# Optimization experiments

Measured on AMD Instinct MI355X. Metric: run time of the kernel, lower is better.

Reference implementation:

```python
import jax, jax.numpy as jnp
import numpy as np

B, LQ, LK, D = 8, 2048, 2048, 1024


def setup_inputs() -> dict:
    key = jax.random.key(0)
    k1, k2, k3, k4, k5 = jax.random.split(key, 5)
    inp = jax.random.normal(k1, (B, LQ, D), dtype=jnp.float32)
    memory = jax.random.normal(k2, (B, LK, D), dtype=jnp.float32)
    # 0/1 float mask over memory positions (1 = masked out)
    mask = (jax.random.uniform(k3, (B, LK)) < 0.15).astype(jnp.float32)
    # nn.Linear(D, 1, bias=False): weight shape [1, D], kaiming-uniform-ish init
    w_input = jax.random.uniform(k4, (1, D), dtype=jnp.float32,
                                 minval=-1.0 / np.sqrt(D), maxval=1.0 / np.sqrt(D))
    # dot_scale ~ U(0, 1/sqrt(D)) per original .uniform_(1/input_size**0.5)
    dot_scale = jax.random.uniform(k5, (D,), dtype=jnp.float32,
                                   minval=0.0, maxval=1.0 / np.sqrt(D))
    return {"input": inp, "memory": memory, "mask": mask,
            "w_input": w_input, "dot_scale": dot_scale}


def reference(input, memory, mask, w_input, dot_scale):
    # input_dot: Linear(D,1,bias=False) -> [B, Lq, 1]
    input_dot = jnp.einsum('bqd,od->bqo', input, w_input)  # o == 1
    # cross_dot: (input * dot_scale) @ memory^T -> [B, Lq, Lk]
    cross_dot = jnp.einsum('bqd,bkd->bqk', input * dot_scale, memory)
    att = input_dot + cross_dot - 1e30 * mask[:, None, :]
    weight_one = jax.nn.softmax(att, axis=-1)  # [B, Lq, Lk]
    output_one = jnp.einsum('bqk,bkd->bqd', weight_one, memory)
    return output_one
```

## Files before the change

### kernel.cpp

```cpp
#include <hip/hip_runtime.h>

#define B_  8
#define LQ_ 2048
#define LK_ 2048
#define D_  1024

typedef unsigned short u16;
using short8  = __attribute__((ext_vector_type(8))) short;
using floatx4 = __attribute__((ext_vector_type(4))) float;

#define GAS __attribute__((address_space(1)))
#define LAS __attribute__((address_space(3)))

__device__ __forceinline__ u16 f2bf(float f) {
  unsigned u = __float_as_uint(f);
  u += 0x7fffu + ((u >> 16) & 1u);
  return (u16)(u >> 16);
}
__device__ __forceinline__ float bf2f(u16 h) {
  return __uint_as_float(((unsigned)h) << 16);
}

__global__ void prep(const float* __restrict__ in, const float* __restrict__ mem,
                     const float* __restrict__ ds, u16* __restrict__ qb,
                     u16* __restrict__ mb, u16* __restrict__ mbT,
                     float* __restrict__ denom) {
  __shared__ u16 tile[64][68];
  int tid = threadIdx.x;
  int tx = tid & 15, ty = tid >> 4;
  int b = blockIdx.z;

  if (denom && blockIdx.y == 16 && blockIdx.x == 0 && blockIdx.z == 0) {
    float4 z = {0.f, 0.f, 0.f, 0.f};
    float4* d4 = (float4*)denom;
#pragma unroll
    for (int i = 0; i < (B_ * LQ_ / 4) / 256; i++)
      d4[tid + i * 256] = z;
  }

  if (blockIdx.y < 16) {
    int k0 = blockIdx.x * 64, d0 = blockIdx.y * 64;
    const float* mB = mem + (size_t)b * LK_ * D_;
    u16* mbB = mb  + (size_t)b * LK_ * D_;
    u16* mtB = mbT + (size_t)b * D_ * LK_;
#pragma unroll
    for (int i = 0; i < 4; i++) {
      int r = ty + 16 * i;
      float4 v = *(const float4*)(mB + (size_t)(k0 + r) * D_ + d0 + tx * 4);
      ushort4 h;
      h.x = f2bf(v.x); h.y = f2bf(v.y); h.z = f2bf(v.z); h.w = f2bf(v.w);
      *(ushort4*)(mbB + (size_t)(k0 + r) * D_ + d0 + tx * 4) = h;
      *(ushort4*)(&tile[r][tx * 4]) = h;
    }
    __syncthreads();
#pragma unroll
    for (int i = 0; i < 4; i++) {
      int rr = ty + 16 * i;
      ushort4 o;
      o.x = tile[tx * 4 + 0][rr];
      o.y = tile[tx * 4 + 1][rr];
      o.z = tile[tx * 4 + 2][rr];
      o.w = tile[tx * 4 + 3][rr];
      *(ushort4*)(mtB + (size_t)(d0 + rr) * LK_ + k0 + tx * 4) = o;
    }
  } else {
    int q0 = blockIdx.x * 64, d0 = (blockIdx.y - 16) * 64;
    const float* iB = in + (size_t)b * LQ_ * D_;
    u16* qB = qb + (size_t)b * LQ_ * D_;
    float4 s4 = *(const float4*)(ds + d0 + tx * 4);
#pragma unroll
    for (int i = 0; i < 4; i++) {
      int r = ty + 16 * i;
      float4 v = *(const float4*)(iB + (size_t)(q0 + r) * D_ + d0 + tx * 4);
      ushort4 h;
      h.x = f2bf(v.x * s4.x); h.y = f2bf(v.y * s4.y);
      h.z = f2bf(v.z * s4.z); h.w = f2bf(v.w * s4.w);
      *(ushort4*)(qB + (size_t)(q0 + r) * D_ + d0 + tx * 4) = h;
    }
  }
}

template <int MODE>
__global__ __launch_bounds__(512, 2) void gemm_bt(
    const u16* __restrict__ A, const u16* __restrict__ Bm,
    void* __restrict__ C, const float* __restrict__ mask,
    float* __restrict__ denom, int K, int ld, int ldc,
    size_t sA, size_t sB, size_t sC) {
  __shared__ __align__(16) u16 As[4 * 8192];
  __shared__ __align__(16) u16 Bs[4 * 8192];

  const int tid = threadIdx.x;
  const int lane = tid & 63, w = tid >> 6;
  const int lm = lane & 15, quad = (lane >> 4) & 3;
  const int wm = (w >> 2) * 128, wn = (w & 3) * 64;

  const int tiles_n = gridDim.x;
  int bid = (blockIdx.z * gridDim.y + blockIdx.y) * tiles_n + blockIdx.x;
  int bz = bid & 7;
  int s = bid >> 3;
  const int GM = 4;
  int per_group = GM * tiles_n;
  int group = s / per_group;
  int rem = s - group * per_group;
  int tm = group * GM + (rem & (GM - 1));
  int tn = rem >> 2;

  const u16* Ab = A  + (size_t)bz * sA + (size_t)(tm * 256) * ld;
  const u16* Bb = Bm + (size_t)bz * sB + (size_t)(tn * 256) * ld;

  int goff[2], ldst[2];
#pragma unroll
  for (int j = 0; j < 2; j++) {
    int c = tid + 512 * j;
    int row = c >> 2;
    int slot = (c & 3) ^ ((row >> 1) & 3);
    goff[j] = row * ld + slot * 8;
    ldst[j] = c * 8;
  }

  const int sw = quad ^ ((lm >> 1) & 3);
  const int aoff = (wm + lm) * 32 + sw * 8;
  const int boff = (wn + lm) * 32 + sw * 8;

  auto stageA = [&](int koff, int plane) {
#pragma unroll
    for (int j = 0; j < 2; j++)
      __builtin_amdgcn_global_load_lds((GAS void*)(Ab + goff[j] + koff),
                                       (LAS void*)(As + (plane << 13) + ldst[j]),
                                       16, 0, 0);
  };
  auto stageB = [&](int koff, int plane) {
#pragma unroll
    for (int j = 0; j < 2; j++)
      __builtin_amdgcn_global_load_lds((GAS void*)(Bb + goff[j] + koff),
                                       (LAS void*)(Bs + (plane << 13) + ldst[j]),
                                       16, 0, 0);
  };

  floatx4 acc[8][4];
#pragma unroll
  for (int i = 0; i < 8; i++)
#pragma unroll
    for (int j = 0; j < 4; j++)
      acc[i][j] = {0.f, 0.f, 0.f, 0.f};

  float rs[8] = {0.f, 0.f, 0.f, 0.f, 0.f, 0.f, 0.f, 0.f};
  short8 bf[4];

#define DS_PHASE(MH, KK, CUR, STG)                                            \
  {                                                                           \
    const u16* Ap = As + (((CUR) * 2 + (KK)) << 13);                          \
    if ((MH) == 0) {                                                          \
      const u16* Bp = Bs + (((CUR) * 2 + (KK)) << 13);                        \
      _Pragma("unroll")                                                       \
      for (int ni = 0; ni < 4; ni++)                                          \
        bf[ni] = *(const short8*)(Bp + boff + ni * 512);                      \
    }                                                                         \
    short8 af[4];                                                             \
    _Pragma("unroll")                                                         \
    for (int m = 0; m < 4; m++)                                               \
      af[m] = *(const short8*)(Ap + aoff + ((MH) * 4 + m) * 512);             \
    STG;                                                                      \
    if constexpr (MODE == 2) {                                                \
      _Pragma("unroll")                                                       \
      for (int m = 0; m < 4; m++) {                                           \
        uint4 u = *(const uint4*)&af[m];                                      \
        rs[(MH) * 4 + m] +=                                                   \
            __uint_as_float(u.x << 16) + __uint_as_float(u.x & 0xffff0000u)   \
          + __uint_as_float(u.y << 16) + __uint_as_float(u.y & 0xffff0000u)   \
          + __uint_as_float(u.z << 16) + __uint_as_float(u.z & 0xffff0000u)   \
          + __uint_as_float(u.w << 16) + __uint_as_float(u.w & 0xffff0000u);  \
      }                                                                       \
    }                                                                         \
    __builtin_amdgcn_s_setprio(1);                                            \
    _Pragma("unroll")                                                         \
    for (int m = 0; m < 4; m++)                                               \
      _Pragma("unroll")                                                       \
      for (int ni = 0; ni < 4; ni++)                                          \
        acc[(MH) * 4 + m][ni] = __builtin_amdgcn_mfma_f32_16x16x32_bf16(      \
            af[m], bf[ni], acc[(MH) * 4 + m][ni], 0, 0, 0);                   \
    __builtin_amdgcn_s_setprio(0);                                            \
  }

  const int NT = K >> 6;
  stageA(0, 0); stageB(0, 0); stageA(32, 1); stageB(32, 1);

  for (int t = 0; t < NT; ++t) {
    const int cur = t & 1, nb = cur ^ 1;
    const bool have = (t + 1 < NT);
    const int k0n = (t + 1) << 6;

    asm volatile("s_waitcnt vmcnt(4)" ::: "memory");
    __builtin_amdgcn_sched_barrier(0);
    __builtin_amdgcn_s_barrier();

    DS_PHASE(0, 0, cur, if (have) stageA(k0n, nb * 2))
    DS_PHASE(1, 0, cur, if (have) stageB(k0n, nb * 2))

    if (have) { asm volatile("s_waitcnt vmcnt(4)" ::: "memory"); }
    else      { asm volatile("s_waitcnt vmcnt(0)" ::: "memory"); }
    __builtin_amdgcn_sched_barrier(0);
    __builtin_amdgcn_s_barrier();

    DS_PHASE(0, 1, cur, if (have) stageA(k0n + 32, nb * 2 + 1))
    DS_PHASE(1, 1, cur, if (have) stageB(k0n + 32, nb * 2 + 1))
  }
#undef DS_PHASE

  const int gm0 = tm * 256 + wm + quad * 4;
  const int gn0 = tn * 256 + wn + lm;
  const size_t cb = (size_t)bz * sC;

  if constexpr (MODE == 1) {
    const float* mrow = mask + (size_t)bz * LK_;
    bool msk[4];
#pragma unroll
    for (int ni = 0; ni < 4; ni++) msk[ni] = (mrow[gn0 + ni * 16] != 0.0f);
#pragma unroll
    for (int mi = 0; mi < 8; mi++) {
#pragma unroll
      for (int r = 0; r < 4; r++) {
        int row = gm0 + mi * 16 + r;
        size_t rowoff = cb + (size_t)row * ldc + gn0;
        float part = 0.f;
#pragma unroll
        for (int ni = 0; ni < 4; ni++) {
          float e = msk[ni] ? 0.f : __expf(acc[mi][ni][r]);
          u16 h = f2bf(e);
          ((u16*)C)[rowoff + ni * 16] = h;
          part += bf2f(h);
        }
        if (denom) {
          part += __shfl_xor(part, 1, 64);
          part += __shfl_xor(part, 2, 64);
          part += __shfl_xor(part, 4, 64);
          part += __shfl_xor(part, 8, 64);
          if (lm == 0) atomicAdd(&denom[(size_t)bz * LQ_ + row], part);
        }
      }
    }
  } else if constexpr (MODE == 0) {
#pragma unroll
    for (int mi = 0; mi < 8; mi++) {
#pragma unroll
      for (int r = 0; r < 4; r++) {
        int row = gm0 + mi * 16 + r;
        float is = 1.0f / denom[(size_t)bz * LQ_ + row];
        size_t rowoff = cb + (size_t)row * ldc + gn0;
#pragma unroll
        for (int ni = 0; ni < 4; ni++)
          ((float*)C)[rowoff + ni * 16] = acc[mi][ni][r] * is;
      }
    }
  } else {
    float inv[8];
#pragma unroll
    for (int mi = 0; mi < 8; mi++) {
      rs[mi] += __shfl_xor(rs[mi], 16, 64);
      rs[mi] += __shfl_xor(rs[mi], 32, 64);
      inv[mi] = 1.0f / rs[mi];
    }
#pragma unroll
    for (int mi = 0; mi < 8; mi++) {
#pragma unroll
      for (int r = 0; r < 4; r++) {
        size_t rowoff = cb + (size_t)(gm0 + mi * 16 + r) * ldc + gn0;
        float is = __shfl(inv[mi], quad * 4 + r, 64);
#pragma unroll
        for (int ni = 0; ni < 4; ni++)
          ((float*)C)[rowoff + ni * 16] = acc[mi][ni][r] * is;
      }
    }
  }
}

extern "C" void kernel_launch(void* const* d_in, const int* in_sizes, int n_in,
                              void* d_out, int out_size, void* d_ws, size_t ws_size,
                              hipStream_t stream) {
  const float* input  = (const float*)d_in[0];
  const float* memory = (const float*)d_in[1];
  const float* mask   = (const float*)d_in[2];
  const float* dscale = (const float*)d_in[4];

  char* ws = (char*)d_ws;
  u16* qb  = (u16*)(ws);
  u16* mb  = (u16*)(ws + (size_t)32 * 1024 * 1024);
  u16* mbT = (u16*)(ws + (size_t)64 * 1024 * 1024);
  u16* E   = (u16*)(ws + (size_t)96 * 1024 * 1024);
  size_t base = (size_t)160 * 1024 * 1024;
  bool have_denom = ws_size >= base + (size_t)B_ * LQ_ * sizeof(float);
  float* denom = have_denom ? (float*)(ws + base) : nullptr;
  float* out = (float*)d_out;

  hipLaunchKernelGGL(prep, dim3(32, 32, B_), dim3(256), 0, stream,
                     input, memory, dscale, qb, mb, mbT, denom);
  hipLaunchKernelGGL((gemm_bt<1>), dim3(LK_ / 256, LQ_ / 256, B_), dim3(512), 0,
                     stream, qb, mb, (void*)E, mask, denom, D_, D_, LK_,
                     (size_t)LQ_ * D_, (size_t)LK_ * D_, (size_t)LQ_ * LK_);
  if (have_denom)
    hipLaunchKernelGGL((gemm_bt<0>), dim3(D_ / 256, LQ_ / 256, B_), dim3(512), 0,
                       stream, E, mbT, (void*)out, nullptr, denom, LK_, LK_, D_,
                       (size_t)LQ_ * LK_, (size_t)D_ * LK_, (size_t)LQ_ * D_);
  else
    hipLaunchKernelGGL((gemm_bt<2>), dim3(D_ / 256, LQ_ / 256, B_), dim3(512), 0,
                       stream, E, mbT, (void*)out, nullptr, nullptr, LK_, LK_, D_,
                       (size_t)LQ_ * LK_, (size_t)D_ * LK_, (size_t)LQ_ * D_);
}
```

Measured before the change: 319.9 us.

## Restructure GEMM main loop to 64-wide K tiles with one barrier per iteration

Changes the LDS layout from two 32-wide K planes per stage to a single 64-wide K tile per buffer with an 8-slot XOR swizzle. The main loop now issues one combined A+B prefetch per iteration and interleaves LDS fragment reads with MFMA groups using lgkmcnt waits. It ends each iteration with a full vmcnt(0) wait and a single barrier, where the old loop had two. This aims to cut barrier and synchronisation overhead, but the load for the next tile must now finish within a single iteration, which can expose memory latency.

```diff
diff --git a/kernel.cpp b/kernel.cpp
--- a/kernel.cpp
+++ b/kernel.cpp
@@ -86,8 +86,8 @@
     void* __restrict__ C, const float* __restrict__ mask,
     float* __restrict__ denom, int K, int ld, int ldc,
     size_t sA, size_t sB, size_t sC) {
-  __shared__ __align__(16) u16 As[4 * 8192];
-  __shared__ __align__(16) u16 Bs[4 * 8192];
+  __shared__ __align__(16) u16 As[2 * 16384];
+  __shared__ __align__(16) u16 Bs[2 * 16384];
 
   const int tid = threadIdx.x;
   const int lane = tid & 63, w = tid >> 6;
@@ -108,104 +108,112 @@
   const u16* Ab = A  + (size_t)bz * sA + (size_t)(tm * 256) * ld;
   const u16* Bb = Bm + (size_t)bz * sB + (size_t)(tn * 256) * ld;
 
-  int goff[2], ldst[2];
-#pragma unroll
-  for (int j = 0; j < 2; j++) {
+  int goff[4], lofs[4];
+#pragma unroll
+  for (int j = 0; j < 4; j++) {
     int c = tid + 512 * j;
-    int row = c >> 2;
-    int slot = (c & 3) ^ ((row >> 1) & 3);
-    goff[j] = row * ld + slot * 8;
-    ldst[j] = c * 8;
-  }
-
-  const int sw = quad ^ ((lm >> 1) & 3);
-  const int aoff = (wm + lm) * 32 + sw * 8;
-  const int boff = (wn + lm) * 32 + sw * 8;
-
-  auto stageA = [&](int koff, int plane) {
-#pragma unroll
-    for (int j = 0; j < 2; j++)
-      __builtin_amdgcn_global_load_lds((GAS void*)(Ab + goff[j] + koff),
-                                       (LAS void*)(As + (plane << 13) + ldst[j]),
+    int rho = c >> 3, sl = c & 7;
+    goff[j] = rho * ld + (sl ^ (rho & 7)) * 8;
+    lofs[j] = c * 8;
+  }
+
+  auto stage = [&](int buf, int k0) {
+#pragma unroll
+    for (int j = 0; j < 4; j++)
+      __builtin_amdgcn_global_load_lds((GAS void*)(Ab + goff[j] + k0),
+                                       (LAS void*)(As + buf * 16384 + lofs[j]),
+                                       16, 0, 0);
+#pragma unroll
+    for (int j = 0; j < 4; j++)
+      __builtin_amdgcn_global_load_lds((GAS void*)(Bb + goff[j] + k0),
+                                       (LAS void*)(Bs + buf * 16384 + lofs[j]),
                                        16, 0, 0);
   };
-  auto stageB = [&](int koff, int plane) {
-#pragma unroll
-    for (int j = 0; j < 2; j++)
-      __builtin_amdgcn_global_load_lds((GAS void*)(Bb + goff[j] + koff),
-                                       (LAS void*)(Bs + (plane << 13) + ldst[j]),
-                                       16, 0, 0);
-  };
-
+
+  const int ka0 = (((0 + quad)) ^ (lm & 7)) * 8;
+  const int ka1 = (((4 + quad)) ^ (lm & 7)) * 8;
+
+  short8 bf[8], afE[4], afO[4];
   floatx4 acc[8][4];
 #pragma unroll
   for (int i = 0; i < 8; i++)
 #pragma unroll
     for (int j = 0; j < 4; j++)
       acc[i][j] = {0.f, 0.f, 0.f, 0.f};
-
   float rs[8] = {0.f, 0.f, 0.f, 0.f, 0.f, 0.f, 0.f, 0.f};
-  short8 bf[4];
-
-#define DS_PHASE(MH, KK, CUR, STG)                                            \
-  {                                                                           \
-    const u16* Ap = As + (((CUR) * 2 + (KK)) << 13);                          \
-    if ((MH) == 0) {                                                          \
-      const u16* Bp = Bs + (((CUR) * 2 + (KK)) << 13);                        \
+
+#define SB __builtin_amdgcn_sched_barrier(0)
+#define LG(N) { asm volatile("s_waitcnt lgkmcnt(" #N ")" ::: "memory"); SB; }
+#define VM0   { asm volatile("s_waitcnt vmcnt(0)" ::: "memory"); SB; }
+
+#define RD_BF(CO)                                                             \
+  { _Pragma("unroll")                                                         \
+    for (int n = 0; n < 4; n++) {                                             \
+      bf[n * 2 + 0] = *(const short8*)(Bs + (CO) + ((wn + n * 16 + lm) << 6) + ka0); \
+      bf[n * 2 + 1] = *(const short8*)(Bs + (CO) + ((wn + n * 16 + lm) << 6) + ka1); \
+    } }
+#define RD_AF(BANK, MP, CO)                                                   \
+  { _Pragma("unroll")                                                         \
+    for (int mi = 0; mi < 2; mi++) {                                          \
+      BANK[mi * 2 + 0] = *(const short8*)(As + (CO) + ((wm + (MP) * 32 + mi * 16 + lm) << 6) + ka0); \
+      BANK[mi * 2 + 1] = *(const short8*)(As + (CO) + ((wm + (MP) * 32 + mi * 16 + lm) << 6) + ka1); \
+    } }
+#define SUMS(BANK, P)                                                         \
+  if constexpr (MODE == 2) {                                                  \
+    _Pragma("unroll")                                                         \
+    for (int mi = 0; mi < 2; mi++)                                            \
       _Pragma("unroll")                                                       \
-      for (int ni = 0; ni < 4; ni++)                                          \
-        bf[ni] = *(const short8*)(Bp + boff + ni * 512);                      \
-    }                                                                         \
-    short8 af[4];                                                             \
-    _Pragma("unroll")                                                         \
-    for (int m = 0; m < 4; m++)                                               \
-      af[m] = *(const short8*)(Ap + aoff + ((MH) * 4 + m) * 512);             \
-    STG;                                                                      \
-    if constexpr (MODE == 2) {                                                \
-      _Pragma("unroll")                                                       \
-      for (int m = 0; m < 4; m++) {                                           \
-        uint4 u = *(const uint4*)&af[m];                                      \
-        rs[(MH) * 4 + m] +=                                                   \
+      for (int ks = 0; ks < 2; ks++) {                                        \
+        uint4 u = *(const uint4*)&BANK[mi * 2 + ks];                          \
+        rs[(P) * 2 + mi] +=                                                   \
             __uint_as_float(u.x << 16) + __uint_as_float(u.x & 0xffff0000u)   \
           + __uint_as_float(u.y << 16) + __uint_as_float(u.y & 0xffff0000u)   \
           + __uint_as_float(u.z << 16) + __uint_as_float(u.z & 0xffff0000u)   \
           + __uint_as_float(u.w << 16) + __uint_as_float(u.w & 0xffff0000u);  \
-      }                                                                       \
-    }                                                                         \
-    __builtin_amdgcn_s_setprio(1);                                            \
+      } }
+#define MM(P, BANK)                                                           \
+  { __builtin_amdgcn_s_setprio(1);                                            \
     _Pragma("unroll")                                                         \
-    for (int m = 0; m < 4; m++)                                               \
+    for (int mi = 0; mi < 2; mi++)                                            \
       _Pragma("unroll")                                                       \
-      for (int ni = 0; ni < 4; ni++)                                          \
-        acc[(MH) * 4 + m][ni] = __builtin_amdgcn_mfma_f32_16x16x32_bf16(      \
-            af[m], bf[ni], acc[(MH) * 4 + m][ni], 0, 0, 0);                   \
-    __builtin_amdgcn_s_setprio(0);                                            \
-  }
+      for (int n = 0; n < 4; n++)                                             \
+        _Pragma("unroll")                                                     \
+        for (int ks = 0; ks < 2; ks++)                                        \
+          acc[(P) * 2 + mi][n] = __builtin_amdgcn_mfma_f32_16x16x32_bf16(     \
+              BANK[mi * 2 + ks], bf[n * 2 + ks], acc[(P) * 2 + mi][n], 0, 0, 0); \
+    __builtin_amdgcn_s_setprio(0); }
 
   const int NT = K >> 6;
-  stageA(0, 0); stageB(0, 0); stageA(32, 1); stageB(32, 1);
+  stage(0, 0);
+  VM0;
+  __builtin_amdgcn_s_barrier();
 
   for (int t = 0; t < NT; ++t) {
-    const int cur = t & 1, nb = cur ^ 1;
+    const int co = (t & 1) * 16384;
+    const int nbuf = (t & 1) ^ 1;
     const bool have = (t + 1 < NT);
-    const int k0n = (t + 1) << 6;
-
-    asm volatile("s_waitcnt vmcnt(4)" ::: "memory");
-    __builtin_amdgcn_sched_barrier(0);
+    const int kn = (t + 1) << 6;
+
+    SB;
+    RD_BF(co) RD_AF(afE, 0, co) RD_AF(afO, 1, co) SB;
+    if (have) stage(nbuf, kn);
+    SB;
+    LG(4)  SUMS(afE, 0) MM(0, afE) SB;
+    RD_AF(afE, 2, co) SB;
+    LG(4)  SUMS(afO, 1) MM(1, afO) SB;
+    RD_AF(afO, 3, co) SB;
+    LG(4)  SUMS(afE, 2) MM(2, afE) SB;
+    LG(0)  SUMS(afO, 3) MM(3, afO) SB;
+    VM0;
     __builtin_amdgcn_s_barrier();
-
-    DS_PHASE(0, 0, cur, if (have) stageA(k0n, nb * 2))
-    DS_PHASE(1, 0, cur, if (have) stageB(k0n, nb * 2))
-
-    if (have) { asm volatile("s_waitcnt vmcnt(4)" ::: "memory"); }
-    else      { asm volatile("s_waitcnt vmcnt(0)" ::: "memory"); }
-    __builtin_amdgcn_sched_barrier(0);
-    __builtin_amdgcn_s_barrier();
-
-    DS_PHASE(0, 1, cur, if (have) stageA(k0n + 32, nb * 2 + 1))
-    DS_PHASE(1, 1, cur, if (have) stageB(k0n + 32, nb * 2 + 1))
-  }
-#undef DS_PHASE
+  }
+#undef MM
+#undef SUMS
+#undef RD_AF
+#undef RD_BF
+#undef LG
+#undef VM0
+#undef SB
 
   const int gm0 = tm * 256 + wm + quad * 4;
   const int gn0 = tn * 256 + wn + lm;
```

Result: no change. 314.1 us (-1.8%).
